# Kernel tuning notes

Measured on AMD Instinct MI355X. Metric: run time of the kernel, lower is better.

Reference implementation:

```python
import jax, jax.numpy as jnp
import numpy as np

B, S, E, D = 64, 2048, 1024, 1024

def setup_inputs() -> dict:
    key = jax.random.key(0)
    ks = jax.random.split(key, 8)
    scale_e = 1.0 / np.sqrt(E)
    scale_d = 1.0 / np.sqrt(D)
    return {
        "encoder_outputs": jax.random.normal(ks[0], (B, S, E), jnp.float32),
        "decoder_hidden": jax.random.normal(ks[1], (B, D), jnp.float32),
        "W1_w": jax.random.normal(ks[2], (E, D), jnp.float32) * scale_e,
        "W1_b": jax.random.normal(ks[3], (D,), jnp.float32) * scale_e,
        "W2_w": jax.random.normal(ks[4], (D, D), jnp.float32) * scale_d,
        "W2_b": jax.random.normal(ks[5], (D,), jnp.float32) * scale_d,
        "V_w": jax.random.normal(ks[6], (D,), jnp.float32) * scale_d,
        "V_b": jnp.zeros((1,), jnp.float32),
    }

def reference(encoder_outputs, decoder_hidden, W1_w, W1_b, W2_w, W2_b, V_w, V_b):
    # proj_enc: [B, S, D]; proj_dec: [B, 1, D] broadcast over src_len
    proj_enc = jnp.einsum("bse,ed->bsd", encoder_outputs, W1_w) + W1_b
    proj_dec = decoder_hidden @ W2_w + W2_b  # [B, D]
    energy = jnp.tanh(proj_enc + proj_dec[:, None, :])  # [B, S, D]
    scores = jnp.einsum("bsd,d->bs", energy, V_w) + V_b[0]  # [B, S]
    attention_weights = jax.nn.softmax(scores, axis=1)  # [B, S]
    context_vector = jnp.einsum("bs,bse->be", attention_weights, encoder_outputs)
    return attention_weights, context_vector
```

## Files before the change

kernel.cpp:

```cpp
#include <hip/hip_runtime.h>

typedef unsigned short u16;
typedef unsigned int   u32;

typedef __attribute__((ext_vector_type(8))) __bf16 bf16x8;
typedef __attribute__((ext_vector_type(4))) float  f32x4;

__device__ __forceinline__ u16 f2bf(float f) {
  union { float f; u32 u; } v; v.f = f;
  return (u16)((v.u + 0x7fffu + ((v.u >> 16) & 1u)) >> 16);
}
__device__ __forceinline__ float bf2f(u16 h) {
  union { u32 u; float f; } v; v.u = ((u32)h) << 16;
  return v.f;
}
__device__ __forceinline__ u32 pk2(float a, float b) {
  return (u32)f2bf(a) | ((u32)f2bf(b) << 16);
}
__device__ __forceinline__ void gl2lds16(const void* g, void* l) {
  __builtin_amdgcn_global_load_lds(
      (const __attribute__((address_space(1))) u32*)g,
      (__attribute__((address_space(3))) u32*)l, 16, 0, 0);
}

__global__ __launch_bounds__(256) void convert_kernel(
    const float* __restrict__ enc, u16* __restrict__ encb) {
  const size_t total = (size_t)131072 * 1024 / 8;
  const size_t stride = (size_t)gridDim.x * 256;
  for (size_t i = (size_t)blockIdx.x * 256 + threadIdx.x; i < total; i += stride) {
    float4 v0 = *reinterpret_cast<const float4*>(enc + i * 8);
    float4 v1 = *reinterpret_cast<const float4*>(enc + i * 8 + 4);
    uint4 o;
    o.x = pk2(v0.x, v0.y); o.y = pk2(v0.z, v0.w);
    o.z = pk2(v1.x, v1.y); o.w = pk2(v1.z, v1.w);
    *reinterpret_cast<uint4*>(encb + i * 8) = o;
  }
}

__global__ __launch_bounds__(256) void transpose_w1_kernel(
    const float* __restrict__ W1, u16* __restrict__ W1s) {
  __shared__ float tile[64][65];
  const int k0 = blockIdx.x * 64, n0 = blockIdx.y * 64;
  const int tx = threadIdx.x & 63, ty = threadIdx.x >> 6;
#pragma unroll
  for (int i = 0; i < 16; ++i) {
    int r = ty + i * 4;
    tile[r][tx] = W1[(k0 + r) * 1024 + n0 + tx];
  }
  __syncthreads();
#pragma unroll
  for (int i = 0; i < 16; ++i) {
    int r = ty * 16 + i;
    int n = n0 + r;
    int k = k0 + tx;
    int kt = k >> 5, kk = k & 31;
    W1s[kt * 32768 + n * 32 + (kk ^ (((n >> 1) & 3) << 3))] = f2bf(tile[tx][r]);
  }
}

__global__ __launch_bounds__(256) void proj_dec_partial(
    const float* __restrict__ dec, const float* __restrict__ W2,
    float* __restrict__ pdp) {
  __shared__ float sdec[64][64];
  const int e0 = blockIdx.x * 64, d0 = blockIdx.y * 64;
  const int dl = threadIdx.x & 63, bg = threadIdx.x >> 6;
#pragma unroll
  for (int i = 0; i < 16; ++i) {
    int flat = threadIdx.x + i * 256;
    sdec[flat >> 6][flat & 63] = dec[(flat >> 6) * 1024 + e0 + (flat & 63)];
  }
  __syncthreads();
  const int d = d0 + dl;
  float acc[16];
#pragma unroll
  for (int i = 0; i < 16; ++i) acc[i] = 0.f;
  for (int e = 0; e < 64; ++e) {
    float w2 = W2[(size_t)(e0 + e) * 1024 + d];
#pragma unroll
    for (int bb = 0; bb < 16; ++bb)
      acc[bb] += sdec[bg * 16 + bb][e] * w2;
  }
#pragma unroll
  for (int bb = 0; bb < 16; ++bb)
    pdp[(size_t)blockIdx.x * 65536 + (size_t)(bg * 16 + bb) * 1024 + d] = acc[bb];
}

__global__ __launch_bounds__(256) void proj_dec_reduce(
    const float* __restrict__ pdp, const float* __restrict__ W2b,
    const float* __restrict__ W1b, float* __restrict__ pd) {
  const int i = blockIdx.x * 256 + threadIdx.x;
  const int d = i & 1023;
  float s = W2b[d] + W1b[d];
#pragma unroll
  for (int j = 0; j < 16; ++j) s += pdp[(size_t)j * 65536 + i];
  pd[i] = s;
}

__global__ __launch_bounds__(256) void proj_dec_kernel(
    const float* __restrict__ dec, const float* __restrict__ W2,
    const float* __restrict__ W2b, const float* __restrict__ W1b,
    float* __restrict__ pd) {
  __shared__ float sdec[16 * 256];
  const int dl = threadIdx.x & 63;
  const int bg = threadIdx.x >> 6;
  const int d  = blockIdx.x * 64 + dl;
  const int b0 = blockIdx.y * 16;
  float acc[4];
#pragma unroll
  for (int i = 0; i < 4; ++i) acc[i] = 0.f;
  for (int et = 0; et < 4; ++et) {
    __syncthreads();
#pragma unroll
    for (int i = 0; i < 16; ++i) {
      int flat = threadIdx.x + i * 256;
      sdec[flat] = dec[(b0 + (flat >> 8)) * 1024 + et * 256 + (flat & 255)];
    }
    __syncthreads();
    for (int e = 0; e < 256; ++e) {
      float w2 = W2[(et * 256 + e) * 1024 + d];
#pragma unroll
      for (int bb = 0; bb < 4; ++bb)
        acc[bb] += sdec[(bg * 4 + bb) * 256 + e] * w2;
    }
  }
  float bias = W2b[d] + W1b[d];
#pragma unroll
  for (int bb = 0; bb < 4; ++bb)
    pd[(b0 + bg * 4 + bb) * 1024 + d] = acc[bb] + bias;
}

__global__ __launch_bounds__(512, 4) void score3_kernel(
    const u16* __restrict__ encb, const u16* __restrict__ W1s,
    const float* __restrict__ pd, const float* __restrict__ Vw,
    float* __restrict__ spart) {
  __shared__ __align__(16) u16 As[3][4096];
  __shared__ __align__(16) u16 Bs[3][8192];
  __shared__ float sc2[8][64];

  const int  tid  = threadIdx.x;
  const int  lane = tid & 63;
  const int  wid  = tid >> 6;
  const int  wm   = wid >> 2, wn = wid & 3;
  const int  l15  = lane & 15, l4 = lane >> 4;
  const int  bid  = blockIdx.x;
  const int  rg   = ((bid >> 5) << 3) | (bid & 7);
  const int  ns   = (bid >> 3) & 3;
  const long row0 = (long)rg * 128;
  const int  b    = rg >> 4;

  const int am  = tid >> 2;
  const int ajx = (tid & 3) ^ ((am >> 1) & 3);
  const u16* abf   = encb + (size_t)(row0 + am) * 1024 + ajx * 8;
  const u16* bbase = W1s + ns * 8192 + tid * 8;

#define STAGE(s, k) do { \
    gl2lds16(abf + (k) * 32, &As[s][tid * 8]); \
    gl2lds16(bbase + (size_t)(k) * 32768, &Bs[s][tid * 8]); \
    gl2lds16(bbase + (size_t)(k) * 32768 + 4096, &Bs[s][4096 + tid * 8]); \
  } while (0)

  f32x4 acc[4][4];
#pragma unroll
  for (int mf = 0; mf < 4; ++mf)
#pragma unroll
    for (int nf = 0; nf < 4; ++nf) acc[mf][nf] = (f32x4){0, 0, 0, 0};

  const int kA = (l4 * 8) ^ (((l15 >> 1) & 3) << 3);

  STAGE(0, 0);
  STAGE(1, 1);
  asm volatile("s_waitcnt vmcnt(3)" ::: "memory");
  __builtin_amdgcn_s_barrier();

#pragma unroll
  for (int kt = 0; kt < 32; ++kt) {
    const int slot = kt % 3;
    const int ps   = (kt + 2) % 3;
    const int pk   = (kt + 2) & 31;
    STAGE(ps, pk);
    asm volatile("s_waitcnt vmcnt(6)" ::: "memory");
    bf16x8 af[4], bf[4];
#pragma unroll
    for (int mf = 0; mf < 4; ++mf)
      af[mf] = *reinterpret_cast<const bf16x8*>(
          &As[slot][(wm * 64 + mf * 16 + l15) * 32 + kA]);
#pragma unroll
    for (int nf = 0; nf < 4; ++nf)
      bf[nf] = *reinterpret_cast<const bf16x8*>(
          &Bs[slot][(wn * 64 + nf * 16 + l15) * 32 + kA]);
    __builtin_amdgcn_s_setprio(1);
#pragma unroll
    for (int nf = 0; nf < 4; ++nf)
#pragma unroll
      for (int mf = 0; mf < 4; ++mf)
        acc[mf][nf] = __builtin_amdgcn_mfma_f32_16x16x32_bf16(af[mf], bf[nf], acc[mf][nf], 0, 0, 0);
    __builtin_amdgcn_s_setprio(0);
    __builtin_amdgcn_s_barrier();
  }
#undef STAGE

  __syncthreads();

  float pd4[4], vw4[4];
#pragma unroll
  for (int nf = 0; nf < 4; ++nf) {
    int c = ns * 256 + wn * 64 + nf * 16 + l15;
    pd4[nf] = pd[b * 1024 + c];
    vw4[nf] = Vw[c];
  }
#pragma unroll
  for (int mf = 0; mf < 4; ++mf)
#pragma unroll
    for (int r = 0; r < 4; ++r) {
      float s = 0.f;
#pragma unroll
      for (int nf = 0; nf < 4; ++nf) {
        float v = acc[mf][nf][r] + pd4[nf];
        float e = __expf(2.f * v);
        s += (1.f - 2.f * __builtin_amdgcn_rcpf(e + 1.f)) * vw4[nf];
      }
      s += __shfl_xor(s, 1);
      s += __shfl_xor(s, 2);
      s += __shfl_xor(s, 4);
      s += __shfl_xor(s, 8);
      if (l15 == 0) sc2[wid][mf * 16 + l4 * 4 + r] = s;
    }
  __syncthreads();
  if (tid < 128) {
    const int wmr = tid >> 6, lr = tid & 63;
    float s = sc2[wmr * 4 + 0][lr] + sc2[wmr * 4 + 1][lr] +
              sc2[wmr * 4 + 2][lr] + sc2[wmr * 4 + 3][lr];
    spart[(size_t)ns * 131072 + row0 + tid] = s;
  }
}

template <int BF>
__global__ __launch_bounds__(512, 4) void score_kernel(
    const float* __restrict__ encf, const u16* __restrict__ encb,
    const u16* __restrict__ W1s, const float* __restrict__ pd,
    const float* __restrict__ Vw, float* __restrict__ spart) {
  __shared__ __align__(16) u16 Bs[2][256 * 32];
  __shared__ __align__(16) u16 As[2][128 * 32];
  __shared__ float sc2[8][64];

  const int  tid  = threadIdx.x;
  const int  lane = tid & 63;
  const int  wid  = tid >> 6;
  const int  wm   = wid >> 2, wn = wid & 3;
  const int  l15  = lane & 15, l4 = lane >> 4;
  const int  bid  = blockIdx.x;
  const int  rg   = ((bid >> 5) << 3) | (bid & 7);
  const int  ns   = (bid >> 3) & 3;
  const long row0 = (long)rg * 128;
  const int  b    = rg >> 4;

  const int am = tid >> 2;
  const int ak8  = (tid & 3) * 8;
  const int aidx = am * 32 + (ak8 ^ (((am >> 1) & 3) << 3));
  const float* aptr = encf + (size_t)(row0 + am) * 1024 + ak8;
  const u16* bbase = W1s + ns * 8192;

  f32x4 acc[4][4];
#pragma unroll
  for (int mf = 0; mf < 4; ++mf)
#pragma unroll
    for (int nf = 0; nf < 4; ++nf) acc[mf][nf] = (f32x4){0, 0, 0, 0};

  const int kA = (l4 * 8) ^ (((l15 >> 1) & 3) << 3);

  {
#pragma unroll
    for (int j = 0; j < 2; ++j)
      gl2lds16(bbase + j * 4096 + tid * 8, &Bs[0][j * 4096 + tid * 8]);
    float4 a0 = *reinterpret_cast<const float4*>(aptr);
    float4 a1 = *reinterpret_cast<const float4*>(aptr + 4);
    uint4 pk;
    pk.x = pk2(a0.x, a0.y); pk.y = pk2(a0.z, a0.w);
    pk.z = pk2(a1.x, a1.y); pk.w = pk2(a1.z, a1.w);
    *reinterpret_cast<uint4*>(&As[0][aidx]) = pk;
  }
  __syncthreads();

  for (int kt = 0; kt < 32; ++kt) {
    const int cur = kt & 1, nxt = cur ^ 1;
    float4 a0, a1;
    if (kt < 31) {
      a0 = *reinterpret_cast<const float4*>(aptr + (kt + 1) * 32);
      a1 = *reinterpret_cast<const float4*>(aptr + (kt + 1) * 32 + 4);
      const u16* bsrc = bbase + (kt + 1) * 32768;
#pragma unroll
      for (int j = 0; j < 2; ++j)
        gl2lds16(bsrc + j * 4096 + tid * 8, &Bs[nxt][j * 4096 + tid * 8]);
    }
    bf16x8 af[4];
#pragma unroll
    for (int mf = 0; mf < 4; ++mf)
      af[mf] = *reinterpret_cast<const bf16x8*>(
          &As[cur][(wm * 64 + mf * 16 + l15) * 32 + kA]);
#pragma unroll
    for (int nf = 0; nf < 4; ++nf) {
      bf16x8 bfr = *reinterpret_cast<const bf16x8*>(
          &Bs[cur][(wn * 64 + nf * 16 + l15) * 32 + kA]);
#pragma unroll
      for (int mf = 0; mf < 4; ++mf)
        acc[mf][nf] = __builtin_amdgcn_mfma_f32_16x16x32_bf16(af[mf], bfr, acc[mf][nf], 0, 0, 0);
    }
    if (kt < 31) {
      uint4 pk;
      pk.x = pk2(a0.x, a0.y); pk.y = pk2(a0.z, a0.w);
      pk.z = pk2(a1.x, a1.y); pk.w = pk2(a1.z, a1.w);
      *reinterpret_cast<uint4*>(&As[nxt][aidx]) = pk;
    }
    __syncthreads();
  }

  float pd4[4], vw4[4];
#pragma unroll
  for (int nf = 0; nf < 4; ++nf) {
    int c = ns * 256 + wn * 64 + nf * 16 + l15;
    pd4[nf] = pd[b * 1024 + c];
    vw4[nf] = Vw[c];
  }
#pragma unroll
  for (int mf = 0; mf < 4; ++mf)
#pragma unroll
    for (int r = 0; r < 4; ++r) {
      float s = 0.f;
#pragma unroll
      for (int nf = 0; nf < 4; ++nf) {
        float v = acc[mf][nf][r] + pd4[nf];
        float e = __expf(2.f * v);
        s += (1.f - 2.f * __builtin_amdgcn_rcpf(e + 1.f)) * vw4[nf];
      }
      s += __shfl_xor(s, 1);
      s += __shfl_xor(s, 2);
      s += __shfl_xor(s, 4);
      s += __shfl_xor(s, 8);
      if (l15 == 0) sc2[wid][mf * 16 + l4 * 4 + r] = s;
    }
  __syncthreads();
  if (tid < 128) {
    const int wmr = tid >> 6, lr = tid & 63;
    float s = sc2[wmr * 4 + 0][lr] + sc2[wmr * 4 + 1][lr] +
              sc2[wmr * 4 + 2][lr] + sc2[wmr * 4 + 3][lr];
    spart[(size_t)ns * 131072 + row0 + tid] = s;
  }
}

__global__ __launch_bounds__(512) void softmax_kernel(
    const float* __restrict__ spart, float* __restrict__ wout) {
  __shared__ float redm[8], reds[8];
  const int b = blockIdx.x, tid = threadIdx.x;
  const size_t base = (size_t)b * 2048 + tid * 4;
  float4 v = *reinterpret_cast<const float4*>(spart + base);
#pragma unroll
  for (int j = 1; j < 4; ++j) {
    float4 p = *reinterpret_cast<const float4*>(spart + (size_t)j * 131072 + base);
    v.x += p.x; v.y += p.y; v.z += p.z; v.w += p.w;
  }
  float m = fmaxf(fmaxf(v.x, v.y), fmaxf(v.z, v.w));
  for (int off = 32; off; off >>= 1) m = fmaxf(m, __shfl_xor(m, off));
  if ((tid & 63) == 0) redm[tid >> 6] = m;
  __syncthreads();
  m = fmaxf(fmaxf(fmaxf(redm[0], redm[1]), fmaxf(redm[2], redm[3])),
            fmaxf(fmaxf(redm[4], redm[5]), fmaxf(redm[6], redm[7])));
  float e0 = __expf(v.x - m), e1 = __expf(v.y - m);
  float e2 = __expf(v.z - m), e3 = __expf(v.w - m);
  float s = e0 + e1 + e2 + e3;
  for (int off = 32; off; off >>= 1) s += __shfl_xor(s, off);
  if ((tid & 63) == 0) reds[tid >> 6] = s;
  __syncthreads();
  s = reds[0] + reds[1] + reds[2] + reds[3] + reds[4] + reds[5] + reds[6] + reds[7];
  float inv = 1.0f / s;
  float4 o; o.x = e0 * inv; o.y = e1 * inv; o.z = e2 * inv; o.w = e3 * inv;
  *reinterpret_cast<float4*>(wout + (size_t)b * 2048 + tid * 4) = o;
}

__global__ __launch_bounds__(256) void context_partial_bf16(
    const float* __restrict__ w, const u16* __restrict__ encb,
    float* __restrict__ cpart) {
  const int b  = blockIdx.x;
  const int ss = blockIdx.y;
  const int e0 = threadIdx.x * 4;
  const u16* ep = encb + ((size_t)b * 2048 + (size_t)ss * 256) * 1024 + e0;
  const float* wp = w + b * 2048 + ss * 256;
  float4 acc = {0, 0, 0, 0};
#pragma unroll 4
  for (int s = 0; s < 256; ++s) {
    ushort4 v = *reinterpret_cast<const ushort4*>(ep + (size_t)s * 1024);
    float ws = wp[s];
    acc.x += ws * bf2f(v.x);
    acc.y += ws * bf2f(v.y);
    acc.z += ws * bf2f(v.z);
    acc.w += ws * bf2f(v.w);
  }
  *reinterpret_cast<float4*>(&cpart[((size_t)(b * 8 + ss)) * 1024 + e0]) = acc;
}

__global__ __launch_bounds__(256) void context_partial_f32(
    const float* __restrict__ w, const float* __restrict__ enc,
    float* __restrict__ cpart) {
  const int b  = blockIdx.x;
  const int es = blockIdx.y;
  const int ss = blockIdx.z;
  const int e  = es * 256 + threadIdx.x;
  const float* ep = enc + ((size_t)b * 2048 + (size_t)ss * 256) * 1024 + e;
  const float* wp = w + b * 2048 + ss * 256;
  float acc = 0.f;
#pragma unroll 8
  for (int s = 0; s < 256; ++s)
    acc += wp[s] * ep[(size_t)s * 1024];
  cpart[((size_t)(b * 8 + ss)) * 1024 + e] = acc;
}

__global__ __launch_bounds__(256) void context_reduce_kernel(
    const float* __restrict__ cpart, float* __restrict__ ctx) {
  const int i = blockIdx.x * 256 + threadIdx.x;
  const int b = i >> 10, e = i & 1023;
  float s = 0.f;
#pragma unroll
  for (int j = 0; j < 8; ++j) s += cpart[(size_t)(b * 8 + j) * 1024 + e];
  ctx[i] = s;
}

extern "C" void kernel_launch(void* const* d_in, const int* in_sizes, int n_in,
                              void* d_out, int out_size, void* d_ws, size_t ws_size,
                              hipStream_t stream) {
  const float* enc = (const float*)d_in[0];
  const float* dec = (const float*)d_in[1];
  const float* W1w = (const float*)d_in[2];
  const float* W1b = (const float*)d_in[3];
  const float* W2w = (const float*)d_in[4];
  const float* W2b = (const float*)d_in[5];
  const float* Vw  = (const float*)d_in[6];

  char* ws = (char*)d_ws;
  float* wout = (float*)d_out;
  float* ctx  = (float*)d_out + 64 * 2048;

  const bool big = ws_size >= ((size_t)263 << 20);
  if (big) {
    u16*   encb  = (u16*)ws;
    u16*   W1s   = (u16*)(ws + ((size_t)256 << 20));
    float* pd    = (float*)(ws + ((size_t)258 << 20));
    char*  shr   = ws + ((size_t)258 << 20) + (256u << 10);
    float* pdp   = (float*)shr;
    float* spart = (float*)shr;
    float* cpart = (float*)(shr + (2u << 20));

    convert_kernel<<<2048, 256, 0, stream>>>(enc, encb);
    transpose_w1_kernel<<<dim3(16, 16), 256, 0, stream>>>(W1w, W1s);
    proj_dec_partial<<<dim3(16, 16), 256, 0, stream>>>(dec, W2w, pdp);
    proj_dec_reduce<<<256, 256, 0, stream>>>(pdp, W2b, W1b, pd);
    score3_kernel<<<4096, 512, 0, stream>>>(encb, W1s, pd, Vw, spart);
    softmax_kernel<<<64, 512, 0, stream>>>(spart, wout);
    context_partial_bf16<<<dim3(64, 8), 256, 0, stream>>>(wout, encb, cpart);
    context_reduce_kernel<<<256, 256, 0, stream>>>(cpart, ctx);
  } else {
    u16*   W1s   = (u16*)ws;
    float* cpart = (float*)ws;
    float* pd    = (float*)(ws + (2u << 20));
    float* spart = (float*)(ws + (2u << 20) + (256u << 10));

    transpose_w1_kernel<<<dim3(16, 16), 256, 0, stream>>>(W1w, W1s);
    proj_dec_kernel<<<dim3(16, 4), 256, 0, stream>>>(dec, W2w, W2b, W1b, pd);
    score_kernel<0><<<4096, 512, 0, stream>>>(enc, (const u16*)nullptr, W1s, pd, Vw, spart);
    softmax_kernel<<<64, 512, 0, stream>>>(spart, wout);
    context_partial_f32<<<dim3(64, 4, 8), 256, 0, stream>>>(wout, enc, cpart);
    context_reduce_kernel<<<256, 256, 0, stream>>>(cpart, ctx);
  }
}
```

Before: 490.9 us.

## Enlarge score GEMM block tile to 256x256 with 1024-thread blocks

The score kernel now gives each 1024-thread block a 256-row by 256-column tile instead of 128 rows, with 16 waves arranged 4x4. Each W1 tile loaded into LDS is therefore reused across twice as many encoder rows, which cuts global and L2 traffic for the weight operand. LDS use rises to about 96KB per block, and a barrier is now added after the wait in every k-step, so 16 waves synchronise twice per iteration. The unused template parameter on the fallback score kernel is also removed.

```diff
diff --git a/kernel.cpp b/kernel.cpp
--- a/kernel.cpp
+++ b/kernel.cpp
@@ -129,35 +129,32 @@
     pd[(b0 + bg * 4 + bb) * 1024 + d] = acc[bb] + bias;
 }
 
-__global__ __launch_bounds__(512, 4) void score3_kernel(
+__global__ __launch_bounds__(1024, 4) void score256_kernel(
     const u16* __restrict__ encb, const u16* __restrict__ W1s,
     const float* __restrict__ pd, const float* __restrict__ Vw,
     float* __restrict__ spart) {
-  __shared__ __align__(16) u16 As[3][4096];
+  __shared__ __align__(16) u16 As[3][8192];
   __shared__ __align__(16) u16 Bs[3][8192];
-  __shared__ float sc2[8][64];
-
-  const int  tid  = threadIdx.x;
-  const int  lane = tid & 63;
-  const int  wid  = tid >> 6;
-  const int  wm   = wid >> 2, wn = wid & 3;
-  const int  l15  = lane & 15, l4 = lane >> 4;
-  const int  bid  = blockIdx.x;
-  const int  rg   = ((bid >> 5) << 3) | (bid & 7);
-  const int  ns   = (bid >> 3) & 3;
-  const long row0 = (long)rg * 128;
-  const int  b    = rg >> 4;
-
-  const int am  = tid >> 2;
-  const int ajx = (tid & 3) ^ ((am >> 1) & 3);
-  const u16* abf   = encb + (size_t)(row0 + am) * 1024 + ajx * 8;
-  const u16* bbase = W1s + ns * 8192 + tid * 8;
+  __shared__ float sc2[16][64];
+
+  const int tid  = threadIdx.x;
+  const int lane = tid & 63;
+  const int wid  = tid >> 6;
+  const int wm = wid >> 2, wn = wid & 3;
+  const int l15 = lane & 15, l4 = lane >> 4;
+  const int bid = blockIdx.x;
+  const int rg  = ((bid >> 5) << 3) | (bid & 7);
+  const int ns  = (bid >> 3) & 3;
+  const long row0 = (long)rg * 256;
+  const int b = rg >> 3;
+
+  const int ar = tid >> 2, aj = tid & 3;
+  const u16* asrc = encb + (size_t)(row0 + ar) * 1024 + ((aj ^ ((ar >> 1) & 3)) << 3);
+  const u16* bsrc = W1s + ns * 8192 + tid * 8;
 
 #define STAGE(s, k) do { \
-    gl2lds16(abf + (k) * 32, &As[s][tid * 8]); \
-    gl2lds16(bbase + (size_t)(k) * 32768, &Bs[s][tid * 8]); \
-    gl2lds16(bbase + (size_t)(k) * 32768 + 4096, &Bs[s][4096 + tid * 8]); \
-  } while (0)
+    gl2lds16(asrc + (k) * 32, &As[s][tid * 8]); \
+    gl2lds16(bsrc + (size_t)(k) * 32768, &Bs[s][tid * 8]); } while (0)
 
   f32x4 acc[4][4];
 #pragma unroll
@@ -169,8 +166,6 @@
 
   STAGE(0, 0);
   STAGE(1, 1);
-  asm volatile("s_waitcnt vmcnt(3)" ::: "memory");
-  __builtin_amdgcn_s_barrier();
 
 #pragma unroll
   for (int kt = 0; kt < 32; ++kt) {
@@ -178,7 +173,8 @@
     const int ps   = (kt + 2) % 3;
     const int pk   = (kt + 2) & 31;
     STAGE(ps, pk);
-    asm volatile("s_waitcnt vmcnt(6)" ::: "memory");
+    asm volatile("s_waitcnt vmcnt(4)" ::: "memory");
+    __builtin_amdgcn_s_barrier();
     bf16x8 af[4], bf[4];
 #pragma unroll
     for (int mf = 0; mf < 4; ++mf)
@@ -226,19 +222,18 @@
       if (l15 == 0) sc2[wid][mf * 16 + l4 * 4 + r] = s;
     }
   __syncthreads();
-  if (tid < 128) {
-    const int wmr = tid >> 6, lr = tid & 63;
-    float s = sc2[wmr * 4 + 0][lr] + sc2[wmr * 4 + 1][lr] +
-              sc2[wmr * 4 + 2][lr] + sc2[wmr * 4 + 3][lr];
+  if (tid < 256) {
+    const int wg = tid >> 6, lr = tid & 63;
+    float s = sc2[wg * 4 + 0][lr] + sc2[wg * 4 + 1][lr] +
+              sc2[wg * 4 + 2][lr] + sc2[wg * 4 + 3][lr];
     spart[(size_t)ns * 131072 + row0 + tid] = s;
   }
 }
 
-template <int BF>
 __global__ __launch_bounds__(512, 4) void score_kernel(
-    const float* __restrict__ encf, const u16* __restrict__ encb,
-    const u16* __restrict__ W1s, const float* __restrict__ pd,
-    const float* __restrict__ Vw, float* __restrict__ spart) {
+    const float* __restrict__ encf, const u16* __restrict__ W1s,
+    const float* __restrict__ pd, const float* __restrict__ Vw,
+    float* __restrict__ spart) {
   __shared__ __align__(16) u16 Bs[2][256 * 32];
   __shared__ __align__(16) u16 As[2][128 * 32];
   __shared__ float sc2[8][64];
@@ -452,7 +447,7 @@
     transpose_w1_kernel<<<dim3(16, 16), 256, 0, stream>>>(W1w, W1s);
     proj_dec_partial<<<dim3(16, 16), 256, 0, stream>>>(dec, W2w, pdp);
     proj_dec_reduce<<<256, 256, 0, stream>>>(pdp, W2b, W1b, pd);
-    score3_kernel<<<4096, 512, 0, stream>>>(encb, W1s, pd, Vw, spart);
+    score256_kernel<<<2048, 1024, 0, stream>>>(encb, W1s, pd, Vw, spart);
     softmax_kernel<<<64, 512, 0, stream>>>(spart, wout);
     context_partial_bf16<<<dim3(64, 8), 256, 0, stream>>>(wout, encb, cpart);
     context_reduce_kernel<<<256, 256, 0, stream>>>(cpart, ctx);
@@ -464,7 +459,7 @@
 
     transpose_w1_kernel<<<dim3(16, 16), 256, 0, stream>>>(W1w, W1s);
     proj_dec_kernel<<<dim3(16, 4), 256, 0, stream>>>(dec, W2w, W2b, W1b, pd);
-    score_kernel<0><<<4096, 512, 0, stream>>>(enc, (const u16*)nullptr, W1s, pd, Vw, spart);
+    score_kernel<<<4096, 512, 0, stream>>>(enc, W1s, pd, Vw, spart);
     softmax_kernel<<<64, 512, 0, stream>>>(spart, wout);
     context_partial_f32<<<dim3(64, 4, 8), 256, 0, stream>>>(wout, enc, cpart);
     context_reduce_kernel<<<256, 256, 0, stream>>>(cpart, ctx);
```

New measurement: 501.6 us. +2.2%, slower.

## Fuse fp32-to-bf16 encoder conversion into first score GEMM N-slice kernel

Applied to the files above, without the earlier changes.

Removes the standalone conversion kernel. A new first-pass score kernel handles N-slice 0: it reads fp32 encoder rows, converts them to bf16 in registers, uses them directly for the MFMA GEMM and writes the bf16 copy to the workspace. A second kernel then handles the other three N-slices from the bf16 copy using the existing triple-buffered pipeline. This saves one full read of the fp32 encoder tensor, at the cost of a less efficient double-buffered register-staged pipeline and an extra launch boundary in the slice-0 kernel.

```diff
diff --git a/kernel.cpp b/kernel.cpp
--- a/kernel.cpp
+++ b/kernel.cpp
@@ -21,20 +21,6 @@
   __builtin_amdgcn_global_load_lds(
       (const __attribute__((address_space(1))) u32*)g,
       (__attribute__((address_space(3))) u32*)l, 16, 0, 0);
-}
-
-__global__ __launch_bounds__(256) void convert_kernel(
-    const float* __restrict__ enc, u16* __restrict__ encb) {
-  const size_t total = (size_t)131072 * 1024 / 8;
-  const size_t stride = (size_t)gridDim.x * 256;
-  for (size_t i = (size_t)blockIdx.x * 256 + threadIdx.x; i < total; i += stride) {
-    float4 v0 = *reinterpret_cast<const float4*>(enc + i * 8);
-    float4 v1 = *reinterpret_cast<const float4*>(enc + i * 8 + 4);
-    uint4 o;
-    o.x = pk2(v0.x, v0.y); o.y = pk2(v0.z, v0.w);
-    o.z = pk2(v1.x, v1.y); o.w = pk2(v1.z, v1.w);
-    *reinterpret_cast<uint4*>(encb + i * 8) = o;
-  }
 }
 
 __global__ __launch_bounds__(256) void transpose_w1_kernel(
@@ -129,12 +115,12 @@
     pd[(b0 + bg * 4 + bb) * 1024 + d] = acc[bb] + bias;
 }
 
-__global__ __launch_bounds__(512, 4) void score3_kernel(
-    const u16* __restrict__ encb, const u16* __restrict__ W1s,
-    const float* __restrict__ pd, const float* __restrict__ Vw,
-    float* __restrict__ spart) {
-  __shared__ __align__(16) u16 As[3][4096];
-  __shared__ __align__(16) u16 Bs[3][8192];
+__global__ __launch_bounds__(512, 4) void score_p1_kernel(
+    const float* __restrict__ encf, u16* __restrict__ encb_out,
+    const u16* __restrict__ W1s, const float* __restrict__ pd,
+    const float* __restrict__ Vw, float* __restrict__ spart) {
+  __shared__ __align__(16) u16 Bs[2][256 * 32];
+  __shared__ __align__(16) u16 As[2][128 * 32];
   __shared__ float sc2[8][64];
 
   const int  tid  = threadIdx.x;
@@ -142,22 +128,16 @@
   const int  wid  = tid >> 6;
   const int  wm   = wid >> 2, wn = wid & 3;
   const int  l15  = lane & 15, l4 = lane >> 4;
-  const int  bid  = blockIdx.x;
-  const int  rg   = ((bid >> 5) << 3) | (bid & 7);
-  const int  ns   = (bid >> 3) & 3;
+  const int  rg   = blockIdx.x;
   const long row0 = (long)rg * 128;
   const int  b    = rg >> 4;
 
-  const int am  = tid >> 2;
-  const int ajx = (tid & 3) ^ ((am >> 1) & 3);
-  const u16* abf   = encb + (size_t)(row0 + am) * 1024 + ajx * 8;
-  const u16* bbase = W1s + ns * 8192 + tid * 8;
-
-#define STAGE(s, k) do { \
-    gl2lds16(abf + (k) * 32, &As[s][tid * 8]); \
-    gl2lds16(bbase + (size_t)(k) * 32768, &Bs[s][tid * 8]); \
-    gl2lds16(bbase + (size_t)(k) * 32768 + 4096, &Bs[s][4096 + tid * 8]); \
-  } while (0)
+  const int am   = tid >> 2;
+  const int ak8  = (tid & 3) * 8;
+  const int aidx = am * 32 + (ak8 ^ (((am >> 1) & 3) << 3));
+  const float* aptr = encf + (size_t)(row0 + am) * 1024 + ak8;
+  u16* wb = encb_out + (size_t)(row0 + am) * 1024 + ak8;
+  const u16* bbase = W1s;
 
   f32x4 acc[4][4];
 #pragma unroll
@@ -167,44 +147,58 @@
 
   const int kA = (l4 * 8) ^ (((l15 >> 1) & 3) << 3);
 
-  STAGE(0, 0);
-  STAGE(1, 1);
-  asm volatile("s_waitcnt vmcnt(3)" ::: "memory");
-  __builtin_amdgcn_s_barrier();
-
-#pragma unroll
+  {
+#pragma unroll
+    for (int j = 0; j < 2; ++j)
+      gl2lds16(bbase + j * 4096 + tid * 8, &Bs[0][j * 4096 + tid * 8]);
+    float4 a0 = *reinterpret_cast<const float4*>(aptr);
+    float4 a1 = *reinterpret_cast<const float4*>(aptr + 4);
+    uint4 pk;
+    pk.x = pk2(a0.x, a0.y); pk.y = pk2(a0.z, a0.w);
+    pk.z = pk2(a1.x, a1.y); pk.w = pk2(a1.z, a1.w);
+    *reinterpret_cast<uint4*>(&As[0][aidx]) = pk;
+    *reinterpret_cast<uint4*>(wb) = pk;
+  }
+  __syncthreads();
+
   for (int kt = 0; kt < 32; ++kt) {
-    const int slot = kt % 3;
-    const int ps   = (kt + 2) % 3;
-    const int pk   = (kt + 2) & 31;
-    STAGE(ps, pk);
-    asm volatile("s_waitcnt vmcnt(6)" ::: "memory");
-    bf16x8 af[4], bf[4];
+    const int cur = kt & 1, nxt = cur ^ 1;
+    float4 a0, a1;
+    if (kt < 31) {
+      a0 = *reinterpret_cast<const float4*>(aptr + (kt + 1) * 32);
+      a1 = *reinterpret_cast<const float4*>(aptr + (kt + 1) * 32 + 4);
+      const u16* bsrc = bbase + (kt + 1) * 32768;
+#pragma unroll
+      for (int j = 0; j < 2; ++j)
+        gl2lds16(bsrc + j * 4096 + tid * 8, &Bs[nxt][j * 4096 + tid * 8]);
+    }
+    bf16x8 af[4];
 #pragma unroll
     for (int mf = 0; mf < 4; ++mf)
       af[mf] = *reinterpret_cast<const bf16x8*>(
-          &As[slot][(wm * 64 + mf * 16 + l15) * 32 + kA]);
-#pragma unroll
-    for (int nf = 0; nf < 4; ++nf)
-      bf[nf] = *reinterpret_cast<const bf16x8*>(
-          &Bs[slot][(wn * 64 + nf * 16 + l15) * 32 + kA]);
-    __builtin_amdgcn_s_setprio(1);
-#pragma unroll
-    for (int nf = 0; nf < 4; ++nf)
+          &As[cur][(wm * 64 + mf * 16 + l15) * 32 + kA]);
+#pragma unroll
+    for (int nf = 0; nf < 4; ++nf) {
+      bf16x8 bfr = *reinterpret_cast<const bf16x8*>(
+          &Bs[cur][(wn * 64 + nf * 16 + l15) * 32 + kA]);
 #pragma unroll
       for (int mf = 0; mf < 4; ++mf)
-        acc[mf][nf] = __builtin_amdgcn_mfma_f32_16x16x32_bf16(af[mf], bf[nf], acc[mf][nf], 0, 0, 0);
-    __builtin_amdgcn_s_setprio(0);
-    __builtin_amdgcn_s_barrier();
-  }
-#undef STAGE
-
-  __syncthreads();
+        acc[mf][nf] = __builtin_amdgcn_mfma_f32_16x16x32_bf16(af[mf], bfr, acc[mf][nf], 0, 0, 0);
+    }
+    if (kt < 31) {
+      uint4 pk;
+      pk.x = pk2(a0.x, a0.y); pk.y = pk2(a0.z, a0.w);
+      pk.z = pk2(a1.x, a1.y); pk.w = pk2(a1.z, a1.w);
+      *reinterpret_cast<uint4*>(&As[nxt][aidx]) = pk;
+      *reinterpret_cast<uint4*>(wb + (kt + 1) * 32) = pk;
+    }
+    __syncthreads();
+  }
 
   float pd4[4], vw4[4];
 #pragma unroll
   for (int nf = 0; nf < 4; ++nf) {
-    int c = ns * 256 + wn * 64 + nf * 16 + l15;
+    int c = wn * 64 + nf * 16 + l15;
     pd4[nf] = pd[b * 1024 + c];
     vw4[nf] = Vw[c];
   }
@@ -230,15 +224,118 @@
     const int wmr = tid >> 6, lr = tid & 63;
     float s = sc2[wmr * 4 + 0][lr] + sc2[wmr * 4 + 1][lr] +
               sc2[wmr * 4 + 2][lr] + sc2[wmr * 4 + 3][lr];
+    spart[row0 + tid] = s;
+  }
+}
+
+__global__ __launch_bounds__(512, 4) void score_p2_kernel(
+    const u16* __restrict__ encb, const u16* __restrict__ W1s,
+    const float* __restrict__ pd, const float* __restrict__ Vw,
+    float* __restrict__ spart) {
+  __shared__ __align__(16) u16 As[3][4096];
+  __shared__ __align__(16) u16 Bs[3][8192];
+  __shared__ float sc2[8][64];
+
+  const int  tid  = threadIdx.x;
+  const int  lane = tid & 63;
+  const int  wid  = tid >> 6;
+  const int  wm   = wid >> 2, wn = wid & 3;
+  const int  l15  = lane & 15, l4 = lane >> 4;
+  const int  rg   = blockIdx.x;
+  const int  ns   = blockIdx.y + 1;
+  const long row0 = (long)rg * 128;
+  const int  b    = rg >> 4;
+
+  const int am  = tid >> 2;
+  const int ajx = (tid & 3) ^ ((am >> 1) & 3);
+  const u16* abf   = encb + (size_t)(row0 + am) * 1024 + ajx * 8;
+  const u16* bbase = W1s + ns * 8192 + tid * 8;
+
+#define STAGE(s, k) do { \
+    gl2lds16(abf + (k) * 32, &As[s][tid * 8]); \
+    gl2lds16(bbase + (size_t)(k) * 32768, &Bs[s][tid * 8]); \
+    gl2lds16(bbase + (size_t)(k) * 32768 + 4096, &Bs[s][4096 + tid * 8]); \
+  } while (0)
+
+  f32x4 acc[4][4];
+#pragma unroll
+  for (int mf = 0; mf < 4; ++mf)
+#pragma unroll
+    for (int nf = 0; nf < 4; ++nf) acc[mf][nf] = (f32x4){0, 0, 0, 0};
+
+  const int kA = (l4 * 8) ^ (((l15 >> 1) & 3) << 3);
+
+  STAGE(0, 0);
+  STAGE(1, 1);
+  asm volatile("s_waitcnt vmcnt(3)" ::: "memory");
+  __builtin_amdgcn_s_barrier();
+
+#pragma unroll
+  for (int kt = 0; kt < 32; ++kt) {
+    const int slot = kt % 3;
+    const int ps   = (kt + 2) % 3;
+    const int pk   = (kt + 2) & 31;
+    STAGE(ps, pk);
+    asm volatile("s_waitcnt vmcnt(6)" ::: "memory");
+    bf16x8 af[4], bf[4];
+#pragma unroll
+    for (int mf = 0; mf < 4; ++mf)
+      af[mf] = *reinterpret_cast<const bf16x8*>(
+          &As[slot][(wm * 64 + mf * 16 + l15) * 32 + kA]);
+#pragma unroll
+    for (int nf = 0; nf < 4; ++nf)
+      bf[nf] = *reinterpret_cast<const bf16x8*>(
+          &Bs[slot][(wn * 64 + nf * 16 + l15) * 32 + kA]);
+    __builtin_amdgcn_s_setprio(1);
+#pragma unroll
+    for (int nf = 0; nf < 4; ++nf)
+#pragma unroll
+      for (int mf = 0; mf < 4; ++mf)
+        acc[mf][nf] = __builtin_amdgcn_mfma_f32_16x16x32_bf16(af[mf], bf[nf], acc[mf][nf], 0, 0, 0);
+    __builtin_amdgcn_s_setprio(0);
+    __builtin_amdgcn_s_barrier();
+  }
+#undef STAGE
+
+  __syncthreads();
+
+  float pd4[4], vw4[4];
+#pragma unroll
+  for (int nf = 0; nf < 4; ++nf) {
+    int c = ns * 256 + wn * 64 + nf * 16 + l15;
+    pd4[nf] = pd[b * 1024 + c];
+    vw4[nf] = Vw[c];
+  }
+#pragma unroll
+  for (int mf = 0; mf < 4; ++mf)
+#pragma unroll
+    for (int r = 0; r < 4; ++r) {
+      float s = 0.f;
+#pragma unroll
+      for (int nf = 0; nf < 4; ++nf) {
+        float v = acc[mf][nf][r] + pd4[nf];
+        float e = __expf(2.f * v);
+        s += (1.f - 2.f * __builtin_amdgcn_rcpf(e + 1.f)) * vw4[nf];
+      }
+      s += __shfl_xor(s, 1);
+      s += __shfl_xor(s, 2);
+      s += __shfl_xor(s, 4);
+      s += __shfl_xor(s, 8);
+      if (l15 == 0) sc2[wid][mf * 16 + l4 * 4 + r] = s;
+    }
+  __syncthreads();
+  if (tid < 128) {
+    const int wmr = tid >> 6, lr = tid & 63;
+    float s = sc2[wmr * 4 + 0][lr] + sc2[wmr * 4 + 1][lr] +
+              sc2[wmr * 4 + 2][lr] + sc2[wmr * 4 + 3][lr];
     spart[(size_t)ns * 131072 + row0 + tid] = s;
   }
 }
 
-template <int BF>
 __global__ __launch_bounds__(512, 4) void score_kernel(
-    const float* __restrict__ encf, const u16* __restrict__ encb,
-    const u16* __restrict__ W1s, const float* __restrict__ pd,
-    const float* __restrict__ Vw, float* __restrict__ spart) {
+    const float* __restrict__ encf, const u16* __restrict__ W1s,
+    const float* __restrict__ pd, const float* __restrict__ Vw,
+    float* __restrict__ spart) {
   __shared__ __align__(16) u16 Bs[2][256 * 32];
   __shared__ __align__(16) u16 As[2][128 * 32];
   __shared__ float sc2[8][64];
@@ -448,11 +545,11 @@
     float* spart = (float*)shr;
     float* cpart = (float*)(shr + (2u << 20));
 
-    convert_kernel<<<2048, 256, 0, stream>>>(enc, encb);
     transpose_w1_kernel<<<dim3(16, 16), 256, 0, stream>>>(W1w, W1s);
     proj_dec_partial<<<dim3(16, 16), 256, 0, stream>>>(dec, W2w, pdp);
     proj_dec_reduce<<<256, 256, 0, stream>>>(pdp, W2b, W1b, pd);
-    score3_kernel<<<4096, 512, 0, stream>>>(encb, W1s, pd, Vw, spart);
+    score_p1_kernel<<<1024, 512, 0, stream>>>(enc, encb, W1s, pd, Vw, spart);
+    score_p2_kernel<<<dim3(1024, 3), 512, 0, stream>>>(encb, W1s, pd, Vw, spart);
     softmax_kernel<<<64, 512, 0, stream>>>(spart, wout);
     context_partial_bf16<<<dim3(64, 8), 256, 0, stream>>>(wout, encb, cpart);
     context_reduce_kernel<<<256, 256, 0, stream>>>(cpart, ctx);
@@ -464,7 +561,7 @@
 
     transpose_w1_kernel<<<dim3(16, 16), 256, 0, stream>>>(W1w, W1s);
     proj_dec_kernel<<<dim3(16, 4), 256, 0, stream>>>(dec, W2w, W2b, W1b, pd);
-    score_kernel<0><<<4096, 512, 0, stream>>>(enc, (const u16*)nullptr, W1s, pd, Vw, spart);
+    score_kernel<<<4096, 512, 0, stream>>>(enc, W1s, pd, Vw, spart);
     softmax_kernel<<<64, 512, 0, stream>>>(spart, wout);
     context_partial_f32<<<dim3(64, 4, 8), 256, 0, stream>>>(wout, enc, cpart);
     context_reduce_kernel<<<256, 256, 0, stream>>>(cpart, ctx);
```

New measurement: 520.5 us. 1.06x slower.
